# Performance work log

Hardware: AMD Instinct MI355X
Metric: run time of the kernel (lower is better)

The kernel has to match this reference:

```python
import jax, jax.numpy as jnp
import numpy as np

EPS = 1e-3  # Keras BatchNormalization default epsilon


def _bn(x, gamma, beta, mean, var):
    # inference-mode batchnorm over channel axis (last)
    inv = gamma * jax.lax.rsqrt(var + EPS)
    return x * inv + (beta - mean * inv)


def setup_inputs() -> dict:
    key = jax.random.key(0)
    ks = jax.random.split(key, 12)
    B, H, W, Cin = 8, 128, 128, 256
    F = 128  # f_g == f_l
    inp = {
        "input_g": jax.random.normal(ks[0], (B, H, W, Cin), jnp.float32),
        "input_x": jax.random.normal(ks[1], (B, H, W, Cin), jnp.float32),
        # w_g branch: 1x1 conv (channel GEMM) + BN
        "Wg": jax.random.normal(ks[2], (Cin, F), jnp.float32) * 0.05,
        "bg": jnp.zeros((F,), jnp.float32),
        "gamma_g": jax.random.uniform(ks[3], (F,), jnp.float32, 0.5, 1.5),
        "beta_g": jax.random.normal(ks[4], (F,), jnp.float32) * 0.1,
        "mean_g": jax.random.normal(ks[5], (F,), jnp.float32) * 0.1,
        "var_g": jax.random.uniform(ks[6], (F,), jnp.float32, 0.5, 1.5),
        # w_x branch
        "Wx": jax.random.normal(ks[7], (Cin, F), jnp.float32) * 0.05,
        "bx": jnp.zeros((F,), jnp.float32),
        "gamma_x": jax.random.uniform(ks[8], (F,), jnp.float32, 0.5, 1.5),
        "beta_x": jax.random.normal(ks[9], (F,), jnp.float32) * 0.1,
        "mean_x": jax.random.normal(ks[10], (F,), jnp.float32) * 0.1,
        "var_x": jax.random.uniform(ks[11], (F,), jnp.float32, 0.5, 1.5),
        # psi: F -> 1 conv + BN + sigmoid
        "Wp": jax.random.normal(jax.random.fold_in(key, 100), (F, 1), jnp.float32) * 0.05,
        "bp": jnp.zeros((1,), jnp.float32),
        "gamma_p": jnp.ones((1,), jnp.float32),
        "beta_p": jnp.zeros((1,), jnp.float32),
        "mean_p": jnp.zeros((1,), jnp.float32),
        "var_p": jnp.ones((1,), jnp.float32),
    }
    return inp


def reference(input_g, input_x, Wg, bg, gamma_g, beta_g, mean_g, var_g,
              Wx, bx, gamma_x, beta_x, mean_x, var_x,
              Wp, bp, gamma_p, beta_p, mean_p, var_p):
    # 1x1 convs are channel contractions: bhwc,cf->bhwf
    g = _bn(jnp.einsum('bhwc,cf->bhwf', input_g, Wg) + bg,
            gamma_g, beta_g, mean_g, var_g)
    x = _bn(jnp.einsum('bhwc,cf->bhwf', input_x, Wx) + bx,
            gamma_x, beta_x, mean_x, var_x)
    s = jax.nn.relu(g + x)                                 # [B,H,W,F]
    psi = jax.nn.sigmoid(_bn(jnp.einsum('bhwf,fo->bhwo', s, Wp) + bp,
                             gamma_p, beta_p, mean_p, var_p))  # [B,H,W,1]
    return x * psi
```

## Files before the change

kernel.cpp:

```cpp
#include <hip/hip_runtime.h>
#include <hip/hip_bf16.h>
#include <math.h>


typedef __bf16 bf16x8 __attribute__((ext_vector_type(8)));
typedef float f32x4 __attribute__((ext_vector_type(4)));

__device__ __forceinline__ unsigned short f2bf(float f) {
  union { float f; unsigned u; } v; v.f = f;
  unsigned r = (v.u + 0x7fffu + ((v.u >> 16) & 1u)) >> 16;
  return (unsigned short)r;
}

__device__ __forceinline__ bf16x8 cvt8(float4 a, float4 b) {
  bf16x8 r;
  r[0]=(__bf16)a.x; r[1]=(__bf16)a.y; r[2]=(__bf16)a.z; r[3]=(__bf16)a.w;
  r[4]=(__bf16)b.x; r[5]=(__bf16)b.y; r[6]=(__bf16)b.z; r[7]=(__bf16)b.w;
  return r;
}

__global__ __launch_bounds__(256) void fold_weights(
    const float* __restrict__ Wg, const float* __restrict__ bg,
    const float* __restrict__ gg, const float* __restrict__ beg,
    const float* __restrict__ mg, const float* __restrict__ vg,
    const float* __restrict__ Wx, const float* __restrict__ bx,
    const float* __restrict__ gx, const float* __restrict__ bex,
    const float* __restrict__ mx, const float* __restrict__ vx,
    const float* __restrict__ Wp, const float* __restrict__ bp,
    const float* __restrict__ gp, const float* __restrict__ bep,
    const float* __restrict__ mp, const float* __restrict__ vp,
    unsigned short* __restrict__ Bfg, unsigned short* __restrict__ Bfx,
    float* __restrict__ cg, float* __restrict__ cx,
    float* __restrict__ wps, float* __restrict__ cps) {
  int idx = blockIdx.x * 256 + threadIdx.x;
  int c = idx >> 7;
  int f = idx & 127;
  float ivg = gg[f] * rsqrtf(vg[f] + 1e-3f);
  float ivx = gx[f] * rsqrtf(vx[f] + 1e-3f);
  int ftile = f >> 4;
  int ksg = c >> 5;
  int lane = (((c >> 3) & 3) << 4) | (f & 15);
  int slot = c & 7;
  int off = ((ftile * 8 + ksg) * 64 + lane) * 8 + slot;
  Bfg[off] = f2bf(Wg[c * 128 + f] * ivg);
  Bfx[off] = f2bf(Wx[c * 128 + f] * ivx);
  if (idx < 128) {
    float ivg2 = gg[idx] * rsqrtf(vg[idx] + 1e-3f);
    float ivx2 = gx[idx] * rsqrtf(vx[idx] + 1e-3f);
    cg[idx] = bg[idx] * ivg2 + beg[idx] - mg[idx] * ivg2;
    cx[idx] = bx[idx] * ivx2 + bex[idx] - mx[idx] * ivx2;
    float ip = gp[0] * rsqrtf(vp[0] + 1e-3f);
    wps[idx] = Wp[idx] * ip;
    if (idx == 0) cps[0] = bp[0] * ip + bep[0] - mp[0] * ip;
  }
}

__global__ __launch_bounds__(512, 4) void attn_gate_main(
    const float* __restrict__ ing, const float* __restrict__ inx,
    const unsigned short* __restrict__ Wfg, const unsigned short* __restrict__ Wfx,
    const float* __restrict__ cgp, const float* __restrict__ cxp,
    const float* __restrict__ wpp, const float* __restrict__ cpp,
    float* __restrict__ out) {
  __shared__ __align__(16) short pixT[2][2][4096];
  __shared__ __align__(16) float xT[2][2048];
  __shared__ __align__(16) float psum[2][16][8];

  const int tid = threadIdx.x;
  const int lane = tid & 63;
  const int wid = tid >> 6;
  const int l15 = lane & 15, l4 = lane >> 4;

  bf16x8 wfg[8], wfx[8];
  #pragma unroll
  for (int ksg = 0; ksg < 8; ++ksg) {
    const int off = ((wid * 8 + ksg) * 64 + lane) * 8;
    wfg[ksg] = *reinterpret_cast<const bf16x8*>(Wfg + off);
    wfx[ksg] = *reinterpret_cast<const bf16x8*>(Wfx + off);
  }
  const int fb = wid * 16 + l4 * 4;
  const f32x4 cgv = *reinterpret_cast<const f32x4*>(cgp + fb);
  const f32x4 cxv = *reinterpret_cast<const f32x4*>(cxp + fb);
  const f32x4 wpv = *reinterpret_cast<const f32x4*>(wpp + fb);
  const float cpsv = cpp[0];

  const int spx = tid >> 5;
  const int sk = tid & 31;
  const int swoff = (spx << 9) | ((sk ^ (spx & 7)) << 4);
  const long tile0 = (long)blockIdx.x * 4;
  const float* gsrc = ing + (tile0 * 16 + spx) * 256 + sk * 8;
  const float* xsrc = inx + (tile0 * 16 + spx) * 256 + sk * 8;

  {
    float4 a0 = *reinterpret_cast<const float4*>(gsrc);
    float4 a1 = *reinterpret_cast<const float4*>(gsrc + 4);
    float4 b0 = *reinterpret_cast<const float4*>(xsrc);
    float4 b1 = *reinterpret_cast<const float4*>(xsrc + 4);
    *reinterpret_cast<bf16x8*>((char*)&pixT[0][0][0] + swoff) = cvt8(a0, a1);
    *reinterpret_cast<bf16x8*>((char*)&pixT[0][1][0] + swoff) = cvt8(b0, b1);
  }
  __syncthreads();

  #pragma unroll
  for (int t = 0; t < 4; ++t) {
    const int buf = t & 1;
    float4 sg0, sg1, sx0, sx1;
    if (t < 3) {
      const float* g_ = gsrc + (t + 1) * 4096;
      const float* x_ = xsrc + (t + 1) * 4096;
      sg0 = *reinterpret_cast<const float4*>(g_);
      sg1 = *reinterpret_cast<const float4*>(g_ + 4);
      sx0 = *reinterpret_cast<const float4*>(x_);
      sx1 = *reinterpret_cast<const float4*>(x_ + 4);
    }

    f32x4 accg = {0.f, 0.f, 0.f, 0.f}, accx = {0.f, 0.f, 0.f, 0.f};
    #pragma unroll
    for (int ksg = 0; ksg < 8; ++ksg) {
      const int ra = (l15 << 9) | ((((ksg << 2) | l4) ^ (l15 & 7)) << 4);
      bf16x8 pg = *reinterpret_cast<const bf16x8*>((const char*)&pixT[buf][0][0] + ra);
      bf16x8 px = *reinterpret_cast<const bf16x8*>((const char*)&pixT[buf][1][0] + ra);
      accg = __builtin_amdgcn_mfma_f32_16x16x32_bf16(wfg[ksg], pg, accg, 0, 0, 0);
      accx = __builtin_amdgcn_mfma_f32_16x16x32_bf16(wfx[ksg], px, accx, 0, 0, 0);
    }

    f32x4 xv;
    float part = 0.f;
    #pragma unroll
    for (int reg = 0; reg < 4; ++reg) {
      float gv = accg[reg] + cgv[reg];
      xv[reg] = accx[reg] + cxv[reg];
      float s = gv + xv[reg];
      s = s > 0.f ? s : 0.f;
      part += s * wpv[reg];
    }
    part += __shfl_xor(part, 16);
    part += __shfl_xor(part, 32);
    if (lane < 16) psum[buf][l15][wid] = part;
    const int xoff = (l15 << 9) | ((((wid << 2) | l4) ^ (l15 & 7)) << 4);
    *reinterpret_cast<f32x4*>((char*)&xT[buf][0] + xoff) = xv;

    if (t < 3) {
      *reinterpret_cast<bf16x8*>((char*)&pixT[buf ^ 1][0][0] + swoff) = cvt8(sg0, sg1);
      *reinterpret_cast<bf16x8*>((char*)&pixT[buf ^ 1][1][0] + swoff) = cvt8(sx0, sx1);
    }

    __syncthreads();

    {
      const f32x4 pa = *reinterpret_cast<const f32x4*>(&psum[buf][spx][0]);
      const f32x4 pb = *reinterpret_cast<const f32x4*>(&psum[buf][spx][4]);
      const float z = pa[0] + pa[1] + pa[2] + pa[3]
                    + pb[0] + pb[1] + pb[2] + pb[3] + cpsv;
      const float psi = 1.f / (1.f + __expf(-z));
      f32x4 xr = *reinterpret_cast<const f32x4*>((const char*)&xT[buf][0] + swoff);
      xr[0] *= psi; xr[1] *= psi; xr[2] *= psi; xr[3] *= psi;
      *reinterpret_cast<f32x4*>(out + ((tile0 + t) * 16 + spx) * 128 + sk * 4) = xr;
    }
  }
}

extern "C" void kernel_launch(void* const* d_in, const int* in_sizes, int n_in,
                              void* d_out, int out_size, void* d_ws, size_t ws_size,
                              hipStream_t stream) {
  const float* ing = (const float*)d_in[0];
  const float* inx = (const float*)d_in[1];
  char* ws = (char*)d_ws;
  unsigned short* Bfg = (unsigned short*)ws;
  unsigned short* Bfx = (unsigned short*)(ws + 65536);
  float* cg  = (float*)(ws + 131072);
  float* cx  = (float*)(ws + 131584);
  float* wps = (float*)(ws + 132096);
  float* cps = (float*)(ws + 132608);

  fold_weights<<<128, 256, 0, stream>>>(
      (const float*)d_in[2],  (const float*)d_in[3],  (const float*)d_in[4],
      (const float*)d_in[5],  (const float*)d_in[6],  (const float*)d_in[7],
      (const float*)d_in[8],  (const float*)d_in[9],  (const float*)d_in[10],
      (const float*)d_in[11], (const float*)d_in[12], (const float*)d_in[13],
      (const float*)d_in[14], (const float*)d_in[15], (const float*)d_in[16],
      (const float*)d_in[17], (const float*)d_in[18], (const float*)d_in[19],
      Bfg, Bfx, cg, cx, wps, cps);

  const int npix = in_sizes[0] / 256;
  const int ntiles = npix / 16;
  attn_gate_main<<<ntiles / 4, 512, 0, stream>>>(
      ing, inx, Bfg, Bfx, cg, cx, wps, cps, (float*)d_out);
}
```

Before: 80.85 us.

## Double pixel tile per block, store x staging as bf16, move prefetch store

Each block now processes 32 pixels per step instead of 16, issuing two MFMAs per weight fragment so the register-resident folded weights are reused across twice as many pixels, and the grid is halved. The x-branch staging buffer in LDS is now packed bf16 with a padded row stride to save LDS space and avoid bank conflicts. The writes of the next tile into LDS move after the output phase, with an extra barrier. The bf16 rounding of x before the psi multiply adds error to the output, and the larger LDS footprint plus higher register pressure may lower occupancy.

```diff
diff --git a/kernel.cpp b/kernel.cpp
--- a/kernel.cpp
+++ b/kernel.cpp
@@ -11,7 +11,9 @@
   unsigned r = (v.u + 0x7fffu + ((v.u >> 16) & 1u)) >> 16;
   return (unsigned short)r;
 }
-
+__device__ __forceinline__ float bf2f(unsigned u) {
+  union { unsigned u; float f; } v; v.u = u << 16; return v.f;
+}
 __device__ __forceinline__ bf16x8 cvt8(float4 a, float4 b) {
   bf16x8 r;
   r[0]=(__bf16)a.x; r[1]=(__bf16)a.y; r[2]=(__bf16)a.z; r[3]=(__bf16)a.w;
@@ -61,9 +63,9 @@
     const float* __restrict__ cgp, const float* __restrict__ cxp,
     const float* __restrict__ wpp, const float* __restrict__ cpp,
     float* __restrict__ out) {
-  __shared__ __align__(16) short pixT[2][2][4096];
-  __shared__ __align__(16) float xT[2][2048];
-  __shared__ __align__(16) float psum[2][16][8];
+  __shared__ __align__(16) short pixT[2][2][8192];
+  __shared__ __align__(16) unsigned short xT[32 * 136];
+  __shared__ __align__(16) float psum[32][8];
 
   const int tid = threadIdx.x;
   const int lane = tid & 63;
@@ -83,78 +85,115 @@
   const f32x4 wpv = *reinterpret_cast<const f32x4*>(wpp + fb);
   const float cpsv = cpp[0];
 
-  const int spx = tid >> 5;
-  const int sk = tid & 31;
-  const int swoff = (spx << 9) | ((sk ^ (spx & 7)) << 4);
+  const int spx = tid >> 4;
+  const int sk = tid & 15;
+  const int sw0 = (spx << 9) | ((sk ^ (spx & 7)) << 4);
+  const int sw1 = (spx << 9) | (((sk + 16) ^ (spx & 7)) << 4);
   const long tile0 = (long)blockIdx.x * 4;
-  const float* gsrc = ing + (tile0 * 16 + spx) * 256 + sk * 8;
-  const float* xsrc = inx + (tile0 * 16 + spx) * 256 + sk * 8;
+  const float* gsrc = ing + (tile0 * 32 + spx) * 256 + sk * 8;
+  const float* xsrc = inx + (tile0 * 32 + spx) * 256 + sk * 8;
 
   {
-    float4 a0 = *reinterpret_cast<const float4*>(gsrc);
-    float4 a1 = *reinterpret_cast<const float4*>(gsrc + 4);
-    float4 b0 = *reinterpret_cast<const float4*>(xsrc);
-    float4 b1 = *reinterpret_cast<const float4*>(xsrc + 4);
-    *reinterpret_cast<bf16x8*>((char*)&pixT[0][0][0] + swoff) = cvt8(a0, a1);
-    *reinterpret_cast<bf16x8*>((char*)&pixT[0][1][0] + swoff) = cvt8(b0, b1);
+    float4 g0 = *reinterpret_cast<const float4*>(gsrc);
+    float4 g1 = *reinterpret_cast<const float4*>(gsrc + 4);
+    float4 g2 = *reinterpret_cast<const float4*>(gsrc + 128);
+    float4 g3 = *reinterpret_cast<const float4*>(gsrc + 132);
+    float4 x0 = *reinterpret_cast<const float4*>(xsrc);
+    float4 x1 = *reinterpret_cast<const float4*>(xsrc + 4);
+    float4 x2 = *reinterpret_cast<const float4*>(xsrc + 128);
+    float4 x3 = *reinterpret_cast<const float4*>(xsrc + 132);
+    *reinterpret_cast<bf16x8*>((char*)&pixT[0][0][0] + sw0) = cvt8(g0, g1);
+    *reinterpret_cast<bf16x8*>((char*)&pixT[0][0][0] + sw1) = cvt8(g2, g3);
+    *reinterpret_cast<bf16x8*>((char*)&pixT[0][1][0] + sw0) = cvt8(x0, x1);
+    *reinterpret_cast<bf16x8*>((char*)&pixT[0][1][0] + sw1) = cvt8(x2, x3);
   }
   __syncthreads();
 
   #pragma unroll
   for (int t = 0; t < 4; ++t) {
     const int buf = t & 1;
-    float4 sg0, sg1, sx0, sx1;
+    float4 pg0, pg1, pg2, pg3, px0, px1, px2, px3;
     if (t < 3) {
-      const float* g_ = gsrc + (t + 1) * 4096;
-      const float* x_ = xsrc + (t + 1) * 4096;
-      sg0 = *reinterpret_cast<const float4*>(g_);
-      sg1 = *reinterpret_cast<const float4*>(g_ + 4);
-      sx0 = *reinterpret_cast<const float4*>(x_);
-      sx1 = *reinterpret_cast<const float4*>(x_ + 4);
-    }
-
-    f32x4 accg = {0.f, 0.f, 0.f, 0.f}, accx = {0.f, 0.f, 0.f, 0.f};
+      const float* g_ = gsrc + (t + 1) * 8192;
+      const float* x_ = xsrc + (t + 1) * 8192;
+      pg0 = *reinterpret_cast<const float4*>(g_);
+      pg1 = *reinterpret_cast<const float4*>(g_ + 4);
+      pg2 = *reinterpret_cast<const float4*>(g_ + 128);
+      pg3 = *reinterpret_cast<const float4*>(g_ + 132);
+      px0 = *reinterpret_cast<const float4*>(x_);
+      px1 = *reinterpret_cast<const float4*>(x_ + 4);
+      px2 = *reinterpret_cast<const float4*>(x_ + 128);
+      px3 = *reinterpret_cast<const float4*>(x_ + 132);
+    }
+
+    f32x4 ag0 = {0.f,0.f,0.f,0.f}, ag1 = {0.f,0.f,0.f,0.f};
+    f32x4 ax0 = {0.f,0.f,0.f,0.f}, ax1 = {0.f,0.f,0.f,0.f};
     #pragma unroll
     for (int ksg = 0; ksg < 8; ++ksg) {
       const int ra = (l15 << 9) | ((((ksg << 2) | l4) ^ (l15 & 7)) << 4);
-      bf16x8 pg = *reinterpret_cast<const bf16x8*>((const char*)&pixT[buf][0][0] + ra);
-      bf16x8 px = *reinterpret_cast<const bf16x8*>((const char*)&pixT[buf][1][0] + ra);
-      accg = __builtin_amdgcn_mfma_f32_16x16x32_bf16(wfg[ksg], pg, accg, 0, 0, 0);
-      accx = __builtin_amdgcn_mfma_f32_16x16x32_bf16(wfx[ksg], px, accx, 0, 0, 0);
-    }
-
-    f32x4 xv;
-    float part = 0.f;
+      const char* bg = (const char*)&pixT[buf][0][0];
+      const char* bx = (const char*)&pixT[buf][1][0];
+      bf16x8 fg0 = *reinterpret_cast<const bf16x8*>(bg + ra);
+      bf16x8 fg1 = *reinterpret_cast<const bf16x8*>(bg + ra + (16 << 9));
+      bf16x8 fx0 = *reinterpret_cast<const bf16x8*>(bx + ra);
+      bf16x8 fx1 = *reinterpret_cast<const bf16x8*>(bx + ra + (16 << 9));
+      ag0 = __builtin_amdgcn_mfma_f32_16x16x32_bf16(wfg[ksg], fg0, ag0, 0, 0, 0);
+      ag1 = __builtin_amdgcn_mfma_f32_16x16x32_bf16(wfg[ksg], fg1, ag1, 0, 0, 0);
+      ax0 = __builtin_amdgcn_mfma_f32_16x16x32_bf16(wfx[ksg], fx0, ax0, 0, 0, 0);
+      ax1 = __builtin_amdgcn_mfma_f32_16x16x32_bf16(wfx[ksg], fx1, ax1, 0, 0, 0);
+    }
+
     #pragma unroll
-    for (int reg = 0; reg < 4; ++reg) {
-      float gv = accg[reg] + cgv[reg];
-      xv[reg] = accx[reg] + cxv[reg];
-      float s = gv + xv[reg];
-      s = s > 0.f ? s : 0.f;
-      part += s * wpv[reg];
-    }
-    part += __shfl_xor(part, 16);
-    part += __shfl_xor(part, 32);
-    if (lane < 16) psum[buf][l15][wid] = part;
-    const int xoff = (l15 << 9) | ((((wid << 2) | l4) ^ (l15 & 7)) << 4);
-    *reinterpret_cast<f32x4*>((char*)&xT[buf][0] + xoff) = xv;
-
-    if (t < 3) {
-      *reinterpret_cast<bf16x8*>((char*)&pixT[buf ^ 1][0][0] + swoff) = cvt8(sg0, sg1);
-      *reinterpret_cast<bf16x8*>((char*)&pixT[buf ^ 1][1][0] + swoff) = cvt8(sx0, sx1);
+    for (int sub = 0; sub < 2; ++sub) {
+      const f32x4 accg = sub ? ag1 : ag0;
+      const f32x4 accx = sub ? ax1 : ax0;
+      float part = 0.f;
+      unsigned pk0, pk1;
+      {
+        float xv0 = accx[0] + cxv[0], xv1 = accx[1] + cxv[1];
+        float xv2 = accx[2] + cxv[2], xv3 = accx[3] + cxv[3];
+        float s0 = (accg[0] + cgv[0]) + xv0; s0 = s0 > 0.f ? s0 : 0.f;
+        float s1 = (accg[1] + cgv[1]) + xv1; s1 = s1 > 0.f ? s1 : 0.f;
+        float s2 = (accg[2] + cgv[2]) + xv2; s2 = s2 > 0.f ? s2 : 0.f;
+        float s3 = (accg[3] + cgv[3]) + xv3; s3 = s3 > 0.f ? s3 : 0.f;
+        part = s0 * wpv[0] + s1 * wpv[1] + s2 * wpv[2] + s3 * wpv[3];
+        pk0 = (unsigned)f2bf(xv0) | ((unsigned)f2bf(xv1) << 16);
+        pk1 = (unsigned)f2bf(xv2) | ((unsigned)f2bf(xv3) << 16);
+      }
+      part += __shfl_xor(part, 16);
+      part += __shfl_xor(part, 32);
+      const int row = l15 + sub * 16;
+      if (lane < 16) psum[row][wid] = part;
+      uint2 pk = {pk0, pk1};
+      *reinterpret_cast<uint2*>((char*)xT + row * 272 + (wid * 4 + l4) * 8) = pk;
     }
 
     __syncthreads();
 
     {
-      const f32x4 pa = *reinterpret_cast<const f32x4*>(&psum[buf][spx][0]);
-      const f32x4 pb = *reinterpret_cast<const f32x4*>(&psum[buf][spx][4]);
+      const int px = tid >> 4, c = tid & 15;
+      const f32x4 pa = *reinterpret_cast<const f32x4*>(&psum[px][0]);
+      const f32x4 pb = *reinterpret_cast<const f32x4*>(&psum[px][4]);
       const float z = pa[0] + pa[1] + pa[2] + pa[3]
                     + pb[0] + pb[1] + pb[2] + pb[3] + cpsv;
       const float psi = 1.f / (1.f + __expf(-z));
-      f32x4 xr = *reinterpret_cast<const f32x4*>((const char*)&xT[buf][0] + swoff);
-      xr[0] *= psi; xr[1] *= psi; xr[2] *= psi; xr[3] *= psi;
-      *reinterpret_cast<f32x4*>(out + ((tile0 + t) * 16 + spx) * 128 + sk * 4) = xr;
+      const uint4 w = *reinterpret_cast<const uint4*>((const char*)xT + px * 272 + c * 16);
+      float4 o0, o1;
+      o0.x = bf2f(w.x & 0xffff) * psi; o0.y = bf2f(w.x >> 16) * psi;
+      o0.z = bf2f(w.y & 0xffff) * psi; o0.w = bf2f(w.y >> 16) * psi;
+      o1.x = bf2f(w.z & 0xffff) * psi; o1.y = bf2f(w.z >> 16) * psi;
+      o1.z = bf2f(w.w & 0xffff) * psi; o1.w = bf2f(w.w >> 16) * psi;
+      float* op = out + ((tile0 + t) * 32 + px) * 128 + c * 8;
+      *reinterpret_cast<float4*>(op) = o0;
+      *reinterpret_cast<float4*>(op + 4) = o1;
+    }
+
+    if (t < 3) {
+      *reinterpret_cast<bf16x8*>((char*)&pixT[buf ^ 1][0][0] + sw0) = cvt8(pg0, pg1);
+      *reinterpret_cast<bf16x8*>((char*)&pixT[buf ^ 1][0][0] + sw1) = cvt8(pg2, pg3);
+      *reinterpret_cast<bf16x8*>((char*)&pixT[buf ^ 1][1][0] + sw0) = cvt8(px0, px1);
+      *reinterpret_cast<bf16x8*>((char*)&pixT[buf ^ 1][1][0] + sw1) = cvt8(px2, px3);
+      __syncthreads();
     }
   }
 }
@@ -182,7 +221,7 @@
       Bfg, Bfx, cg, cx, wps, cps);
 
   const int npix = in_sizes[0] / 256;
-  const int ntiles = npix / 16;
+  const int ntiles = npix / 32;
   attn_gate_main<<<ntiles / 4, 512, 0, stream>>>(
       ing, inx, Bfg, Bfx, cg, cx, wps, cps, (float*)d_out);
 }
```

Measured after the change: 110.2 us. 1.36x slower.
